# Performance work log

Measured on AMD Instinct MI355X. Metric: run time of the kernel, lower is better.

Reference implementation:

```python
import jax, jax.numpy as jnp
import numpy as np

N = 100000
EPS = 1e-16  # PyG softmax denominator epsilon

def _gat_layer(x, ei, W, a_src, a_dst, bias, heads, ch, concat):
    # x: [N, Fin]; ei: [2, E] (self-loops already included)
    h = (x @ W).reshape(N, heads, ch)              # [N, H, C]
    alpha_s = jnp.sum(h * a_src, axis=-1)           # [N, H]
    alpha_d = jnp.sum(h * a_dst, axis=-1)           # [N, H]
    src, dst = ei[0], ei[1]
    e = alpha_s[src] + alpha_d[dst]                 # [E, H]
    e = jax.nn.leaky_relu(e, negative_slope=0.2)
    # segment softmax over incoming edges of each dst node
    m = jax.ops.segment_max(e, dst, num_segments=N)
    e = jnp.exp(e - m[dst])
    s = jax.ops.segment_sum(e, dst, num_segments=N)
    alpha = e / (s[dst] + EPS)                      # [E, H]
    msg = h[src] * alpha[:, :, None]                # [E, H, C]
    out = jax.ops.segment_sum(msg, dst, num_segments=N)  # [N, H, C]
    if concat:
        out = out.reshape(N, heads * ch)
    else:
        out = out.mean(axis=1)
    return out + bias

def _add_self_loops(edge_index):
    loops = jnp.arange(N, dtype=edge_index.dtype)
    return jnp.concatenate([edge_index, jnp.stack([loops, loops])], axis=1)

def setup_inputs() -> dict:
    key = jax.random.key(0)
    ks = jax.random.split(key, 12)
    in_ch, hid, out_ch, H = 64, 32, 8, 4
    E = 1_600_000
    x = jax.random.normal(ks[0], (N, in_ch), dtype=jnp.float32)
    edge_index = jax.random.randint(ks[1], (2, E), 0, N, dtype=jnp.int64)
    sc1 = 1.0 / np.sqrt(in_ch)
    sc2 = 1.0 / np.sqrt(hid * H)
    scl = 1.0 / np.sqrt(hid)
    return {
        "x": x,
        "W1": jax.random.normal(ks[2], (in_ch, H * hid), dtype=jnp.float32) * sc1,
        "a_src1": jax.random.normal(ks[3], (H, hid), dtype=jnp.float32) * scl,
        "a_dst1": jax.random.normal(ks[4], (H, hid), dtype=jnp.float32) * scl,
        "b1": jnp.zeros((H * hid,), dtype=jnp.float32),
        "W2": jax.random.normal(ks[5], (H * hid, hid), dtype=jnp.float32) * sc2,
        "a_src2": jax.random.normal(ks[6], (1, hid), dtype=jnp.float32) * scl,
        "a_dst2": jax.random.normal(ks[7], (1, hid), dtype=jnp.float32) * scl,
        "b2": jnp.zeros((hid,), dtype=jnp.float32),
        "Wl": jax.random.normal(ks[8], (hid, out_ch), dtype=jnp.float32) * scl,
        "bl": jnp.zeros((out_ch,), dtype=jnp.float32),
        "edge_index": edge_index,
    }

def reference(x, W1, a_src1, a_dst1, b1, W2, a_src2, a_dst2, b2, Wl, bl, edge_index):
    ei = _add_self_loops(edge_index)
    hid, H = 32, 4
    h = _gat_layer(x, ei, W1, a_src1, a_dst1, b1, H, hid, concat=True)
    h = jax.nn.relu(h)
    # dropout p=0.3 is identity in eval mode
    h = _gat_layer(h, ei, W2, a_src2, a_dst2, b2, 1, hid, concat=True)
    h = jax.nn.relu(h)
    return h @ Wl + bl
```

## Files before the change

kernel.cpp:

```cpp
#include <hip/hip_runtime.h>
#include <hip/hip_fp16.h>

#define NNODES 100000
#define H1 4
#define C1 32
#define F0 64
#define F1 128
#define C2 32
#define FOUT 8
#define SCAN_B 1024
#define NB 98
#define BCAP 64

__device__ __forceinline__ float lrelu(float v) {
    return v > 0.f ? v : 0.2f * v;
}


__global__ void k_binit(int* slots) {
    int n = blockIdx.x * blockDim.x + threadIdx.x;
    if (n >= NNODES) return;
    *(int2*)(slots + (size_t)n * BCAP) = make_int2(2, n);
}

__global__ void k_bfill(const int* __restrict__ ei, int E, int* slots) {
    int e = blockIdx.x * blockDim.x + threadIdx.x;
    if (e >= E) return;
    int s = ei[e];
    int d = ei[E + e];
    int p = atomicAdd(&slots[(size_t)d * BCAP], 1);
    slots[(size_t)d * BCAP + p] = s;
}


__global__ void k_zero(int* rowptr) {
    int i = blockIdx.x * blockDim.x + threadIdx.x;
    if (i < NNODES) rowptr[i] = 1;
}

__global__ void k_deg(const int* __restrict__ ei, int E, int* rowptr) {
    int e0 = (blockIdx.x * blockDim.x + threadIdx.x) * 4;
    if (e0 >= E) return;
    int4 d = *(const int4*)(ei + E + e0);
    atomicAdd(&rowptr[d.x], 1);
    atomicAdd(&rowptr[d.y], 1);
    atomicAdd(&rowptr[d.z], 1);
    atomicAdd(&rowptr[d.w], 1);
}

__global__ __launch_bounds__(SCAN_B) void k_scan_local(int* rowptr, int* bsum) {
    __shared__ int tmp[SCAN_B];
    int t = threadIdx.x;
    int i = blockIdx.x * SCAN_B + t;
    int v = (i < NNODES) ? rowptr[i] : 0;
    tmp[t] = v;
    for (int off = 1; off < SCAN_B; off <<= 1) {
        __syncthreads();
        int x = (t >= off) ? tmp[t - off] : 0;
        __syncthreads();
        tmp[t] += x;
    }
    __syncthreads();
    if (i < NNODES) rowptr[i] = tmp[t] - v;
    if (t == SCAN_B - 1) bsum[blockIdx.x] = tmp[t];
}

__global__ void k_scan_carry(int* bsum) {
    __shared__ int tmp[128];
    int t = threadIdx.x;
    tmp[t] = (t < NB) ? bsum[t] : 0;
    __syncthreads();
    if (t == 0) {
        int acc = 0;
        for (int b = 0; b < NB; b++) { int v = tmp[b]; tmp[b] = acc; acc += v; }
    }
    __syncthreads();
    if (t < NB) bsum[t] = tmp[t];
}

__global__ void k_scan_add(int* rowptr, const int* __restrict__ bsum) {
    int i = blockIdx.x * blockDim.x + threadIdx.x;
    if (i < NNODES) rowptr[i] += bsum[i >> 10];
}

__global__ void k_fill_self(int* rowptr, int* adj) {
    int n = blockIdx.x * blockDim.x + threadIdx.x;
    if (n >= NNODES) return;
    int pos = atomicAdd(&rowptr[n], 1);
    adj[pos] = n;
}

__global__ void k_fill(const int* __restrict__ ei, int E, int* rowptr, int* adj) {
    int e0 = (blockIdx.x * blockDim.x + threadIdx.x) * 4;
    if (e0 >= E) return;
    int4 s = *(const int4*)(ei + e0);
    int4 d = *(const int4*)(ei + E + e0);
    int p0 = atomicAdd(&rowptr[d.x], 1);
    int p1 = atomicAdd(&rowptr[d.y], 1);
    int p2 = atomicAdd(&rowptr[d.z], 1);
    int p3 = atomicAdd(&rowptr[d.w], 1);
    adj[p0] = s.x; adj[p1] = s.y; adj[p2] = s.z; adj[p3] = s.w;
}


__global__ __launch_bounds__(256) void k_gemm1(const float* __restrict__ x,
                                               const float* __restrict__ W1,
                                               __half* __restrict__ h1h) {
    __shared__ float wl[F0 * F1];
    __shared__ float xs[32 * F0];
    int t = threadIdx.x;
    int row0 = blockIdx.x * 32;
    for (int i = t; i < F0 * F1; i += 256) wl[i] = W1[i];
    for (int i = t; i < 32 * F0; i += 256) xs[i] = x[(size_t)row0 * F0 + i];
    __syncthreads();
    int c2 = t & 63;
    int g = t >> 6;
    float a0[8], a1[8];
#pragma unroll
    for (int i = 0; i < 8; i++) { a0[i] = 0.f; a1[i] = 0.f; }
    for (int k = 0; k < F0; k++) {
        float w0 = wl[k * F1 + 2 * c2];
        float w1 = wl[k * F1 + 2 * c2 + 1];
#pragma unroll
        for (int i = 0; i < 8; i++) {
            float xv = xs[(g * 8 + i) * F0 + k];
            a0[i] += xv * w0;
            a1[i] += xv * w1;
        }
    }
#pragma unroll
    for (int i = 0; i < 8; i++) {
        int row = row0 + g * 8 + i;
        *(__half2*)(h1h + (size_t)row * F1 + 2 * c2) = __floats2half2_rn(a0[i], a1[i]);
    }
}

__global__ void k_att1(const __half* __restrict__ h1h, const float* __restrict__ a_src,
                       const float* __restrict__ a_dst, float* as1, float* ad1) {
    int i = blockIdx.x * blockDim.x + threadIdx.x;
    if (i >= NNODES * H1) return;
    int h = i & 3;
    const __half2* hv = (const __half2*)(h1h + (size_t)(i >> 2) * F1 + h * C1);
    float s = 0.f, d = 0.f;
#pragma unroll
    for (int c = 0; c < C1 / 2; c++) {
        float2 v = __half22float2(hv[c]);
        s += v.x * a_src[h * C1 + 2 * c] + v.y * a_src[h * C1 + 2 * c + 1];
        d += v.x * a_dst[h * C1 + 2 * c] + v.y * a_dst[h * C1 + 2 * c + 1];
    }
    as1[i] = s; ad1[i] = d;
}

__global__ __launch_bounds__(256) void k_agg1(const int* __restrict__ idx,
                                              const int* __restrict__ rowptr,
                                              const int* __restrict__ cnt,
                                              const float* __restrict__ as1,
                                              const float* __restrict__ ad1,
                                              const __half* __restrict__ h1h,
                                              const float* __restrict__ b1,
                                              float* __restrict__ out1) {
    __shared__ float red[2][2][16][8];
    __shared__ float sred[2][2][16];
    int t = threadIdx.x;
    int nl = t >> 7;
    int n = blockIdx.x * 2 + nl;
    int u = t & 127;
    int slot = u >> 4;
    int c = u & 15;
    int h = c >> 2;
    int start, end;
    if (cnt) {
        int cur = cnt[(size_t)n * BCAP];
        start = n * BCAP + 1; end = n * BCAP + cur;
    } else {
        start = (n == 0) ? 0 : rowptr[n - 1]; end = rowptr[n];
    }
    float adv = ad1[n * 4 + h];
    float acc[8];
#pragma unroll
    for (int i = 0; i < 8; i++) acc[i] = 0.f;
    float sacc = 0.f;
#pragma unroll 2
    for (int k = start + slot; k < end; k += 8) {
        int src = idx[k];
        float w = __expf(lrelu(as1[src * 4 + h] + adv));
        float4 raw = *(const float4*)(h1h + (size_t)src * F1 + c * 8);
        const __half2* hp = (const __half2*)&raw;
#pragma unroll
        for (int q = 0; q < 4; q++) {
            float2 f = __half22float2(hp[q]);
            acc[2 * q]     += w * f.x;
            acc[2 * q + 1] += w * f.y;
        }
        sacc += w;
    }
#pragma unroll
    for (int mask = 16; mask <= 32; mask <<= 1) {
#pragma unroll
        for (int i = 0; i < 8; i++) acc[i] += __shfl_xor(acc[i], mask);
        sacc += __shfl_xor(sacc, mask);
    }
    if ((u & 48) == 0) {
        int wv = u >> 6;
#pragma unroll
        for (int i = 0; i < 8; i++) red[nl][wv][c][i] = acc[i];
        sred[nl][wv][c] = sacc;
    }
    __syncthreads();
    if (u < 16) {
        float s = sred[nl][0][u] + sred[nl][1][u];
        float rs = 1.f / (s + 1e-16f);
        float o[8];
#pragma unroll
        for (int i = 0; i < 8; i++) {
            float a = red[nl][0][u][i] + red[nl][1][u][i];
            float v = a * rs + b1[u * 8 + i];
            o[i] = v > 0.f ? v : 0.f;
        }
        float* dst = out1 + (size_t)n * F1 + u * 8;
        *(float4*)(dst)     = make_float4(o[0], o[1], o[2], o[3]);
        *(float4*)(dst + 4) = make_float4(o[4], o[5], o[6], o[7]);
    }
}

__global__ __launch_bounds__(256) void k_gemm2(const float* __restrict__ xin,
                                               const float* __restrict__ W2,
                                               __half* __restrict__ h2h) {
    __shared__ float wl[F1 * C2];
    __shared__ float xs[64 * F1];
    int t = threadIdx.x;
    int row0 = blockIdx.x * 64;
    for (int i = t; i < F1 * C2; i += 256) wl[i] = W2[i];
    for (int i = t; i < 64 * F1; i += 256) {
        int r = i >> 7, k = i & 127;
        int row = row0 + r;
        xs[i] = (row < NNODES) ? xin[(size_t)row * F1 + k] : 0.f;
    }
    __syncthreads();
    int c2 = t & 15;
    int g = t >> 4;
    float a0[4], a1[4];
#pragma unroll
    for (int i = 0; i < 4; i++) { a0[i] = 0.f; a1[i] = 0.f; }
    for (int k = 0; k < F1; k++) {
        float w0 = wl[k * C2 + 2 * c2];
        float w1 = wl[k * C2 + 2 * c2 + 1];
#pragma unroll
        for (int i = 0; i < 4; i++) {
            float xv = xs[(g * 4 + i) * F1 + k];
            a0[i] += xv * w0;
            a1[i] += xv * w1;
        }
    }
#pragma unroll
    for (int i = 0; i < 4; i++) {
        int row = row0 + g * 4 + i;
        if (row < NNODES)
            *(__half2*)(h2h + (size_t)row * C2 + 2 * c2) = __floats2half2_rn(a0[i], a1[i]);
    }
}

__global__ void k_att2(const __half* __restrict__ h2h, const float* __restrict__ a_src,
                       const float* __restrict__ a_dst, float* as2, float* ad2) {
    int n = blockIdx.x * blockDim.x + threadIdx.x;
    if (n >= NNODES) return;
    const __half2* hv = (const __half2*)(h2h + (size_t)n * C2);
    float s = 0.f, d = 0.f;
#pragma unroll
    for (int c = 0; c < C2 / 2; c++) {
        float2 v = __half22float2(hv[c]);
        s += v.x * a_src[2 * c] + v.y * a_src[2 * c + 1];
        d += v.x * a_dst[2 * c] + v.y * a_dst[2 * c + 1];
    }
    as2[n] = s; ad2[n] = d;
}

__global__ __launch_bounds__(256) void k_agg2f(const int* __restrict__ idx,
                                               const int* __restrict__ rowptr,
                                               const int* __restrict__ cnt,
                                               const float* __restrict__ as2,
                                               const float* __restrict__ ad2,
                                               const __half* __restrict__ h2h,
                                               const float* __restrict__ b2,
                                               const float* __restrict__ Wl,
                                               const float* __restrict__ bl,
                                               float* __restrict__ out) {
    int t = threadIdx.x;
    int n = blockIdx.x * 8 + (t >> 5);
    int u = t & 31;
    int slot = u >> 3;
    int c = u & 7;
    int start, end;
    if (cnt) {
        int cur = cnt[(size_t)n * BCAP];
        start = n * BCAP + 1; end = n * BCAP + cur;
    } else {
        start = (n == 0) ? 0 : rowptr[n - 1]; end = rowptr[n];
    }
    float adv = ad2[n];
    float4 acc = make_float4(0.f, 0.f, 0.f, 0.f);
    float sacc = 0.f;
#pragma unroll 2
    for (int k = start + slot; k < end; k += 4) {
        int src = idx[k];
        float w = __expf(lrelu(as2[src] + adv));
        const __half2* hp = (const __half2*)(h2h + (size_t)src * C2 + c * 4);
        float2 f0 = __half22float2(hp[0]);
        float2 f1 = __half22float2(hp[1]);
        acc.x += w * f0.x; acc.y += w * f0.y;
        acc.z += w * f1.x; acc.w += w * f1.y;
        sacc += w;
    }
#pragma unroll
    for (int mask = 8; mask <= 16; mask <<= 1) {
        acc.x += __shfl_xor(acc.x, mask);
        acc.y += __shfl_xor(acc.y, mask);
        acc.z += __shfl_xor(acc.z, mask);
        acc.w += __shfl_xor(acc.w, mask);
        sacc  += __shfl_xor(sacc, mask);
    }
    if (slot == 0) {
        float rs = 1.f / (sacc + 1e-16f);
        float4 bv = *(const float4*)(b2 + c * 4);
        float4 o;
        o.x = acc.x * rs + bv.x; o.y = acc.y * rs + bv.y;
        o.z = acc.z * rs + bv.z; o.w = acc.w * rs + bv.w;
        o.x = o.x > 0.f ? o.x : 0.f;
        o.y = o.y > 0.f ? o.y : 0.f;
        o.z = o.z > 0.f ? o.z : 0.f;
        o.w = o.w > 0.f ? o.w : 0.f;
        float p[FOUT];
#pragma unroll
        for (int j = 0; j < FOUT; j++) {
            p[j] = o.x * Wl[(4 * c + 0) * FOUT + j]
                 + o.y * Wl[(4 * c + 1) * FOUT + j]
                 + o.z * Wl[(4 * c + 2) * FOUT + j]
                 + o.w * Wl[(4 * c + 3) * FOUT + j];
        }
#pragma unroll
        for (int mask = 1; mask <= 4; mask <<= 1) {
#pragma unroll
            for (int j = 0; j < FOUT; j++) p[j] += __shfl_xor(p[j], mask);
        }
        out[(size_t)n * FOUT + c] = p[c] + bl[c];
    }
}

extern "C" void kernel_launch(void* const* d_in, const int* in_sizes, int n_in,
                              void* d_out, int out_size, void* d_ws, size_t ws_size,
                              hipStream_t stream) {
    const float* x      = (const float*)d_in[0];
    const float* W1     = (const float*)d_in[1];
    const float* a_src1 = (const float*)d_in[2];
    const float* a_dst1 = (const float*)d_in[3];
    const float* b1     = (const float*)d_in[4];
    const float* W2     = (const float*)d_in[5];
    const float* a_src2 = (const float*)d_in[6];
    const float* a_dst2 = (const float*)d_in[7];
    const float* b2     = (const float*)d_in[8];
    const float* Wl     = (const float*)d_in[9];
    const float* bl     = (const float*)d_in[10];
    const int*   ei     = (const int*)d_in[11];
    int E = in_sizes[11] / 2;
    int Etot = E + NNODES;
    float* out = (float*)d_out;

    __half* h1h  = (__half*)d_ws;
    float* out1  = (float*)(h1h + (size_t)NNODES * F1);
    float* as1   = out1 + (size_t)NNODES * F1;
    float* ad1   = as1 + (size_t)NNODES * H1;
    int*   ibase = (int*)(ad1 + (size_t)NNODES * H1);
    __half* h2h = h1h;
    float* as2 = as1;
    float* ad2 = ad1;

    size_t need_bucket = (size_t)NNODES * F1 * 2 + (size_t)NNODES * F1 * 4
                       + (size_t)NNODES * H1 * 8
                       + (size_t)NNODES * BCAP * 4;
    bool bucket = (ws_size >= need_bucket);

    const int B = 256;
    if (bucket) {
        int* slots = ibase;
        k_binit<<<(NNODES + B - 1) / B, B, 0, stream>>>(slots);
        k_bfill<<<(E + B - 1) / B, B, 0, stream>>>(ei, E, slots);
        k_gemm1<<<NNODES / 32, B, 0, stream>>>(x, W1, h1h);
        k_att1<<<(NNODES * H1 + B - 1) / B, B, 0, stream>>>(h1h, a_src1, a_dst1, as1, ad1);
        k_agg1<<<NNODES / 2, B, 0, stream>>>(slots, nullptr, slots, as1, ad1, h1h, b1, out1);
        k_gemm2<<<(NNODES + 63) / 64, B, 0, stream>>>(out1, W2, h2h);
        k_att2<<<(NNODES + B - 1) / B, B, 0, stream>>>(h2h, a_src2, a_dst2, as2, ad2);
        k_agg2f<<<NNODES / 8, B, 0, stream>>>(slots, nullptr, slots, as2, ad2, h2h, b2, Wl, bl, out);
    } else {
        int* adj    = ibase;
        int* rowptr = adj + (size_t)Etot;
        int* bsum   = rowptr + NNODES;
        k_zero<<<(NNODES + B - 1) / B, B, 0, stream>>>(rowptr);
        k_deg<<<(E / 4 + B - 1) / B, B, 0, stream>>>(ei, E, rowptr);
        k_scan_local<<<NB, SCAN_B, 0, stream>>>(rowptr, bsum);
        k_scan_carry<<<1, 128, 0, stream>>>(bsum);
        k_scan_add<<<(NNODES + B - 1) / B, B, 0, stream>>>(rowptr, bsum);
        k_fill_self<<<(NNODES + B - 1) / B, B, 0, stream>>>(rowptr, adj);
        k_fill<<<(E / 4 + B - 1) / B, B, 0, stream>>>(ei, E, rowptr, adj);
        k_gemm1<<<NNODES / 32, B, 0, stream>>>(x, W1, h1h);
        k_att1<<<(NNODES * H1 + B - 1) / B, B, 0, stream>>>(h1h, a_src1, a_dst1, as1, ad1);
        k_agg1<<<NNODES / 2, B, 0, stream>>>(adj, rowptr, nullptr, as1, ad1, h1h, b1, out1);
        k_gemm2<<<(NNODES + 63) / 64, B, 0, stream>>>(out1, W2, h2h);
        k_att2<<<(NNODES + B - 1) / B, B, 0, stream>>>(h2h, a_src2, a_dst2, as2, ad2);
        k_agg2f<<<NNODES / 8, B, 0, stream>>>(adj, rowptr, nullptr, as2, ad2, h2h, b2, Wl, bl, out);
    }
}
```

Measured before the change: 301.9 us.

## Fuse bucket fill with GEMM1 and attention logits into single launches

Merges the edge-bucket fill, the first-layer GEMM and the first attention-logit computation into one kernel. Blocks are split by index, so the GEMM blocks run concurrently with the atomic scatter blocks. Attention dot products are computed from the GEMM accumulators via warp shuffles, which removes separate att1/att2 kernels and their re-reads of h. W1 is staged in shared memory as half2 to shrink LDS use, but this adds rounding to the GEMM weights and mixes heterogeneous block types in one launch.

```diff
diff --git a/kernel.cpp b/kernel.cpp
--- a/kernel.cpp
+++ b/kernel.cpp
@@ -23,13 +23,80 @@
     *(int2*)(slots + (size_t)n * BCAP) = make_int2(2, n);
 }
 
-__global__ void k_bfill(const int* __restrict__ ei, int E, int* slots) {
-    int e = blockIdx.x * blockDim.x + threadIdx.x;
-    if (e >= E) return;
-    int s = ei[e];
-    int d = ei[E + e];
-    int p = atomicAdd(&slots[(size_t)d * BCAP], 1);
-    slots[(size_t)d * BCAP + p] = s;
+__global__ __launch_bounds__(256) void k_fused1(const int* __restrict__ ei, int E,
+                                                int* slots,
+                                                const float* __restrict__ x,
+                                                const float* __restrict__ W1,
+                                                const float* __restrict__ a_src1,
+                                                const float* __restrict__ a_dst1,
+                                                __half* __restrict__ h1h,
+                                                float* __restrict__ as1,
+                                                float* __restrict__ ad1,
+                                                int ngemm) {
+    __shared__ __half2 wl[F0 * 64];
+    __shared__ float xs[32 * F0];
+    if ((int)blockIdx.x >= ngemm) {
+        int e = ((int)blockIdx.x - ngemm) * 256 + threadIdx.x;
+        if (e >= E) return;
+        int s = ei[e];
+        int d = ei[E + e];
+        int p = atomicAdd(&slots[(size_t)d * BCAP], 1);
+        slots[(size_t)d * BCAP + p] = s;
+        return;
+    }
+    int t = threadIdx.x;
+    int row0 = blockIdx.x * 32;
+    for (int i = t; i < F0 * 64; i += 256) {
+        int k = i >> 6, c = i & 63;
+        wl[i] = __floats2half2_rn(W1[k * F1 + 2 * c], W1[k * F1 + 2 * c + 1]);
+    }
+    for (int i = t; i < 32 * F0; i += 256) xs[i] = x[(size_t)row0 * F0 + i];
+    __syncthreads();
+    int c2 = t & 63;
+    int g = t >> 6;
+    float a0[8], a1[8];
+#pragma unroll
+    for (int i = 0; i < 8; i++) { a0[i] = 0.f; a1[i] = 0.f; }
+    for (int k = 0; k < F0; k++) {
+        float2 w = __half22float2(wl[k * 64 + c2]);
+#pragma unroll
+        for (int i = 0; i < 8; i++) {
+            float xv = xs[(g * 8 + i) * F0 + k];
+            a0[i] += xv * w.x;
+            a1[i] += xv * w.y;
+        }
+    }
+#pragma unroll
+    for (int i = 0; i < 8; i++) {
+        int row = row0 + g * 8 + i;
+        *(__half2*)(h1h + (size_t)row * F1 + 2 * c2) = __floats2half2_rn(a0[i], a1[i]);
+    }
+    int h = c2 >> 4;
+    int cc = 2 * (c2 & 15);
+    float s0 = a_src1[h * C1 + cc], s1 = a_src1[h * C1 + cc + 1];
+    float d0 = a_dst1[h * C1 + cc], d1 = a_dst1[h * C1 + cc + 1];
+    float sp[8], dp[8];
+#pragma unroll
+    for (int i = 0; i < 8; i++) {
+        sp[i] = a0[i] * s0 + a1[i] * s1;
+        dp[i] = a0[i] * d0 + a1[i] * d1;
+    }
+#pragma unroll
+    for (int mask = 1; mask <= 8; mask <<= 1) {
+#pragma unroll
+        for (int i = 0; i < 8; i++) {
+            sp[i] += __shfl_xor(sp[i], mask);
+            dp[i] += __shfl_xor(dp[i], mask);
+        }
+    }
+    if ((c2 & 15) == 0) {
+#pragma unroll
+        for (int i = 0; i < 8; i++) {
+            int row = row0 + g * 8 + i;
+            as1[row * 4 + h] = sp[i];
+            ad1[row * 4 + h] = dp[i];
+        }
+    }
 }
 
 
@@ -101,7 +168,6 @@
     int p3 = atomicAdd(&rowptr[d.w], 1);
     adj[p0] = s.x; adj[p1] = s.y; adj[p2] = s.z; adj[p3] = s.w;
 }
-
 
 __global__ __launch_bounds__(256) void k_gemm1(const float* __restrict__ x,
                                                const float* __restrict__ W1,
@@ -223,9 +289,13 @@
     }
 }
 
-__global__ __launch_bounds__(256) void k_gemm2(const float* __restrict__ xin,
-                                               const float* __restrict__ W2,
-                                               __half* __restrict__ h2h) {
+__global__ __launch_bounds__(256) void k_gemm2a(const float* __restrict__ xin,
+                                                const float* __restrict__ W2,
+                                                const float* __restrict__ a_src2,
+                                                const float* __restrict__ a_dst2,
+                                                __half* __restrict__ h2h,
+                                                float* __restrict__ as2,
+                                                float* __restrict__ ad2) {
     __shared__ float wl[F1 * C2];
     __shared__ float xs[64 * F1];
     int t = threadIdx.x;
@@ -257,6 +327,29 @@
         int row = row0 + g * 4 + i;
         if (row < NNODES)
             *(__half2*)(h2h + (size_t)row * C2 + 2 * c2) = __floats2half2_rn(a0[i], a1[i]);
+    }
+    float s0 = a_src2[2 * c2], s1 = a_src2[2 * c2 + 1];
+    float d0 = a_dst2[2 * c2], d1 = a_dst2[2 * c2 + 1];
+    float sp[4], dp[4];
+#pragma unroll
+    for (int i = 0; i < 4; i++) {
+        sp[i] = a0[i] * s0 + a1[i] * s1;
+        dp[i] = a0[i] * d0 + a1[i] * d1;
+    }
+#pragma unroll
+    for (int mask = 1; mask <= 8; mask <<= 1) {
+#pragma unroll
+        for (int i = 0; i < 4; i++) {
+            sp[i] += __shfl_xor(sp[i], mask);
+            dp[i] += __shfl_xor(dp[i], mask);
+        }
+    }
+    if (c2 == 0) {
+#pragma unroll
+        for (int i = 0; i < 4; i++) {
+            int row = row0 + g * 4 + i;
+            if (row < NNODES) { as2[row] = sp[i]; ad2[row] = dp[i]; }
+        }
     }
 }
 
@@ -382,13 +475,13 @@
     const int B = 256;
     if (bucket) {
         int* slots = ibase;
+        int ngemm = NNODES / 32;
+        int nbfill = (E + B - 1) / B;
         k_binit<<<(NNODES + B - 1) / B, B, 0, stream>>>(slots);
-        k_bfill<<<(E + B - 1) / B, B, 0, stream>>>(ei, E, slots);
-        k_gemm1<<<NNODES / 32, B, 0, stream>>>(x, W1, h1h);
-        k_att1<<<(NNODES * H1 + B - 1) / B, B, 0, stream>>>(h1h, a_src1, a_dst1, as1, ad1);
+        k_fused1<<<ngemm + nbfill, B, 0, stream>>>(ei, E, slots, x, W1,
+                                                   a_src1, a_dst1, h1h, as1, ad1, ngemm);
         k_agg1<<<NNODES / 2, B, 0, stream>>>(slots, nullptr, slots, as1, ad1, h1h, b1, out1);
-        k_gemm2<<<(NNODES + 63) / 64, B, 0, stream>>>(out1, W2, h2h);
-        k_att2<<<(NNODES + B - 1) / B, B, 0, stream>>>(h2h, a_src2, a_dst2, as2, ad2);
+        k_gemm2a<<<(NNODES + 63) / 64, B, 0, stream>>>(out1, W2, a_src2, a_dst2, h2h, as2, ad2);
         k_agg2f<<<NNODES / 8, B, 0, stream>>>(slots, nullptr, slots, as2, ad2, h2h, b2, Wl, bl, out);
     } else {
         int* adj    = ibase;
@@ -404,8 +497,7 @@
         k_gemm1<<<NNODES / 32, B, 0, stream>>>(x, W1, h1h);
         k_att1<<<(NNODES * H1 + B - 1) / B, B, 0, stream>>>(h1h, a_src1, a_dst1, as1, ad1);
         k_agg1<<<NNODES / 2, B, 0, stream>>>(adj, rowptr, nullptr, as1, ad1, h1h, b1, out1);
-        k_gemm2<<<(NNODES + 63) / 64, B, 0, stream>>>(out1, W2, h2h);
-        k_att2<<<(NNODES + B - 1) / B, B, 0, stream>>>(h2h, a_src2, a_dst2, as2, ad2);
+        k_gemm2a<<<(NNODES + 63) / 64, B, 0, stream>>>(out1, W2, a_src2, a_dst2, h2h, as2, ad2);
         k_agg2f<<<NNODES / 8, B, 0, stream>>>(adj, rowptr, nullptr, as2, ad2, h2h, b2, Wl, bl, out);
     }
 }
```

Measured after the change: 278.8 us. 7.6% less time.
